# Performance work log

Hardware: AMD Instinct MI355X
Metric: run time of the kernel (lower is better)

The kernel has to match this reference:

```python
import jax, jax.numpy as jnp
import numpy as np

B, T, C, H = 2, 2048, 1024, 16
HS = C // H  # head size = 64


def _rope_cos_sin(t, hs):
    # theta_i = 1/10000^(2(i-1)/hs) for i in [1, hs/2]
    pos = jnp.arange(t, dtype=jnp.float32)[:, None]          # [T,1]
    i = jnp.arange(1, hs // 2 + 1, dtype=jnp.float32)[None]  # [1,hs/2]
    theta = 1.0 / 10000.0 ** (2.0 * (i - 1.0) / hs)
    ang = pos * theta                                        # [T,hs/2]
    return jnp.cos(ang), jnp.sin(ang)


def _apply_rope(u, cos, sin):
    # u: [B,H,T,HS]; complex multiply on consecutive pairs
    u2 = u.reshape(*u.shape[:-1], HS // 2, 2)
    x0, x1 = u2[..., 0], u2[..., 1]
    c = cos[None, None]  # [1,1,T,hs/2]
    s = sin[None, None]
    r0 = x0 * c - x1 * s
    r1 = x0 * s + x1 * c
    return jnp.stack([r0, r1], axis=-1).reshape(u.shape)


def setup_inputs() -> dict:
    key = jax.random.key(0)
    ks = jax.random.split(key, 5)
    return {
        "x": jax.random.normal(ks[0], (B, T, C), dtype=jnp.float32),
        "W_qkv": jax.random.normal(ks[1], (C, 3 * C), dtype=jnp.float32) * 0.02,
        "b_qkv": jax.random.normal(ks[2], (3 * C,), dtype=jnp.float32) * 0.02,
        "W_proj": jax.random.normal(ks[3], (C, C), dtype=jnp.float32) * 0.02,
        "b_proj": jax.random.normal(ks[4], (C,), dtype=jnp.float32) * 0.02,
    }


def reference(x, W_qkv, b_qkv, W_proj, b_proj):
    b, t, c = x.shape
    qkv = x @ W_qkv + b_qkv                                   # [B,T,3C]
    qkv = qkv.reshape(b, t, H, 3 * HS).transpose(0, 2, 1, 3)  # [B,H,T,3*HS]
    q, k, v = jnp.split(qkv, 3, axis=-1)                      # each [B,H,T,HS]

    cos, sin = _rope_cos_sin(t, HS)
    q = _apply_rope(q, cos, sin)
    k = _apply_rope(k, cos, sin)

    att = jnp.einsum("bhqd,bhkd->bhqk", q, k) / jnp.sqrt(jnp.float32(HS))
    causal = jnp.tril(jnp.ones((t, t), dtype=bool))[None, None]
    att = jnp.where(causal, att, jnp.float32(-1e9))
    att = jax.nn.softmax(att, axis=-1)
    y = jnp.einsum("bhqk,bhkd->bhqd", att, v)                 # [B,H,T,HS]
    y = y.transpose(0, 2, 1, 3).reshape(b, t, c)
    return y @ W_proj + b_proj
```

## Files before the change

### kernel.cpp

```cpp
#include <hip/hip_runtime.h>

typedef unsigned short u16;
typedef unsigned int u32;
typedef __bf16 bf16x8 __attribute__((ext_vector_type(8)));
typedef float f32x4 __attribute__((ext_vector_type(4)));
typedef u16 u16x4 __attribute__((ext_vector_type(4)));
typedef u16 u16x8 __attribute__((ext_vector_type(8)));

__device__ __forceinline__ u16 f2bf(float f) {
  u32 u = __builtin_bit_cast(u32, f);
  u += 0x7fffu + ((u >> 16) & 1u);
  return (u16)(u >> 16);
}

__device__ __forceinline__ u32 pk2(float a, float b) {
  u32 ua = __builtin_bit_cast(u32, a) + 0x8000u;
  u32 ub = __builtin_bit_cast(u32, b) + 0x8000u;
  return __builtin_amdgcn_perm(ub, ua, 0x07060302);
}

__device__ __forceinline__ void gld16(const void* g, void* l) {
  __builtin_amdgcn_global_load_lds(
      (const __attribute__((address_space(1))) void*)g,
      (__attribute__((address_space(3))) void*)l, 16, 0, 0);
}

__global__ __launch_bounds__(256) void k_prep(
    const float* __restrict__ x, u16* __restrict__ xb,
    const float* __restrict__ Wqkv, u16* __restrict__ Wqkvt,
    const float* __restrict__ Wproj, u16* __restrict__ Wpt,
    float2* __restrict__ rope) {
  __shared__ float tile[32][33];
  const int tid = threadIdx.x;
  int bx = blockIdx.x;
  if (bx < 4096) {
    int i = (bx * 256 + tid) * 4;
    float4 v = *(const float4*)(x + i);
    u16x4 o = { f2bf(v.x), f2bf(v.y), f2bf(v.z), f2bf(v.w) };
    *(u16x4*)(xb + i) = o;
    return;
  }
  bx -= 4096;
  const float* src; u16* dst; int R, Cc, bxx, byy;
  if (bx < 3072) {
    src = Wqkv; dst = Wqkvt; R = 1024; Cc = 3072; bxx = bx % 96; byy = bx / 96;
  } else if (bx < 4096) {
    int b = bx - 3072;
    src = Wproj; dst = Wpt; R = 1024; Cc = 1024; bxx = b % 32; byy = b / 32;
  } else {
    int i = (bx - 4096) * 256 + tid;
    int t = i >> 5, d = i & 31;
    float theta = expf(-(float)d * 0.28782313662425575f);
    float ang = (float)t * theta;
    rope[i] = make_float2(cosf(ang), sinf(ang));
    return;
  }
  int xx = tid & 31, yy = tid >> 5;
  int c0 = bxx * 32, r0 = byy * 32;
  for (int i = 0; i < 4; ++i)
    tile[yy + 8 * i][xx] = src[(size_t)(r0 + yy + 8 * i) * Cc + c0 + xx];
  __syncthreads();
  for (int i = 0; i < 4; ++i)
    dst[(size_t)(c0 + yy + 8 * i) * R + r0 + xx] = f2bf(tile[xx][yy + 8 * i]);
}

__global__ __launch_bounds__(256, 4) void k_qkv(
    const u16* __restrict__ Xb,
    const u16* __restrict__ Wt,
    const float* __restrict__ bias,
    const float2* __restrict__ rope,
    u16* __restrict__ Qg,
    u16* __restrict__ Kg,
    u16* __restrict__ Vt) {
  __shared__ alignas(16) u16 smem[18432];
  u16* As = smem;
  u16* Bs = smem + 8192;
  const int tid = threadIdx.x;
  const int lane = tid & 63, w = tid >> 6;
  const int quad = lane >> 4, l15 = lane & 15;
  const int m0 = blockIdx.y * 128, n0 = blockIdx.x * 128;
  const int wm = (w & 1) * 64, wn = (w >> 1) * 64;
  const int srow = lane >> 3, sj = lane & 7;
  const int sw = (sj ^ srow) * 8;
  const f32x4 vzero = {0.f, 0.f, 0.f, 0.f};

  f32x4 acc[4][4];
  for (int i = 0; i < 4; ++i)
    for (int j = 0; j < 4; ++j) acc[i][j] = vzero;

  for (int kt = 0; kt < 1024; kt += 64) {
    __syncthreads();
    for (int i = 0; i < 4; ++i) {
      int row = w * 32 + i * 8;
      gld16(Xb + (size_t)(m0 + row + srow) * 1024 + kt + sw, &As[row * 64]);
      gld16(Wt + (size_t)(n0 + row + srow) * 1024 + kt + sw, &Bs[row * 64]);
    }
    __syncthreads();
    for (int ks = 0; ks < 2; ++ks) {
      const int cc = ((ks * 4 + quad) ^ (l15 & 7)) * 8;
      bf16x8 a[4], b[4];
      for (int mt = 0; mt < 4; ++mt)
        a[mt] = *(const bf16x8*)&As[(wm + mt * 16 + l15) * 64 + cc];
      for (int nt = 0; nt < 4; ++nt)
        b[nt] = *(const bf16x8*)&Bs[(wn + nt * 16 + l15) * 64 + cc];
      for (int nt = 0; nt < 4; ++nt)
        for (int mt = 0; mt < 4; ++mt)
          acc[nt][mt] = __builtin_amdgcn_mfma_f32_16x16x32_bf16(
              b[nt], a[mt], acc[nt][mt], 0, 0, 0);
    }
  }
  __syncthreads();

  const int half = w >> 1;
  const int nh = n0 + half * 64;
  const int region = (nh % 192) >> 6;
  u16* Eh = smem + half * 9216;
  if (region < 2) {
    const float qsc = (region == 0) ? 0.18033688011112042f : 1.0f;
    for (int nt = 0; nt < 4; ++nt) {
      float4 bv4 = *(const float4*)&bias[nh + nt * 16 + quad * 4];
      for (int mt = 0; mt < 4; ++mt) {
        int m_l = wm + mt * 16 + l15;
        int t = (m0 + m_l) & 2047;
        float4 cs = *(const float4*)&rope[t * 32 + nt * 8 + quad * 2];
        float v0 = acc[nt][mt][0] + bv4.x;
        float v1 = acc[nt][mt][1] + bv4.y;
        float v2 = acc[nt][mt][2] + bv4.z;
        float v3 = acc[nt][mt][3] + bv4.w;
        float r0 = fmaf(-v1, cs.y, v0 * cs.x) * qsc;
        float r1 = fmaf( v0, cs.y, v1 * cs.x) * qsc;
        float r2 = fmaf(-v3, cs.w, v2 * cs.z) * qsc;
        float r3 = fmaf( v2, cs.w, v3 * cs.z) * qsc;
        uint2 pv; pv.x = pk2(r0, r1); pv.y = pk2(r2, r3);
        *(uint2*)&Eh[m_l * 72 + nt * 16 + quad * 4] = pv;
      }
    }
  } else {
    for (int nt = 0; nt < 4; ++nt) {
      float4 bv4 = *(const float4*)&bias[nh + nt * 16 + quad * 4];
      for (int mt = 0; mt < 4; ++mt) {
        int m_l = wm + mt * 16 + l15;
        int cb = nt * 16 + quad * 4;
        Eh[(cb + 0) * 136 + m_l] = f2bf(acc[nt][mt][0] + bv4.x);
        Eh[(cb + 1) * 136 + m_l] = f2bf(acc[nt][mt][1] + bv4.y);
        Eh[(cb + 2) * 136 + m_l] = f2bf(acc[nt][mt][2] + bv4.z);
        Eh[(cb + 3) * 136 + m_l] = f2bf(acc[nt][mt][3] + bv4.w);
      }
    }
  }
  __syncthreads();

  const int bb = m0 >> 11, t0 = m0 & 2047;
  for (int hf = 0; hf < 2; ++hf) {
    const int nhf = n0 + hf * 64;
    const int hh = nhf / 192;
    const int reg = (nhf % 192) >> 6;
    const u16* Ef = smem + hf * 9216;
    if (reg < 2) {
      u16* dst = (reg == 0 ? Qg : Kg) +
                 ((size_t)(bb * 16 + hh) * 2048 + t0) * 64;
      int chunk = tid & 7, row0 = tid >> 3;
      for (int p = 0; p < 4; ++p) {
        int row = row0 + p * 32;
        u16x8 val = *(const u16x8*)&Ef[row * 72 + chunk * 8];
        *(u16x8*)(dst + (size_t)row * 64 + chunk * 8) = val;
      }
    } else {
      u16* dstv = Vt + (size_t)(bb * 16 + hh) * 64 * 2048 + t0;
      int mch = tid & 15, c0r = tid >> 4;
      for (int p = 0; p < 4; ++p) {
        int c = c0r + p * 16;
        u16x8 val = *(const u16x8*)&Ef[c * 136 + mch * 8];
        *(u16x8*)(dstv + (size_t)c * 2048 + mch * 8) = val;
      }
    }
  }
}

__global__ __launch_bounds__(256, 4) void k_attn(
    const u16* __restrict__ Qg, const u16* __restrict__ Kg,
    const u16* __restrict__ Vt, u16* __restrict__ Og) {
  __shared__ alignas(16) u16 Ks[2][64 * 64];
  __shared__ alignas(16) u16 Vs[2][64 * 64];
  __shared__ alignas(16) u16 Ps[64 * 64];
  const int tid = threadIdx.x, lane = tid & 63, w = tid >> 6;
  const int quad = lane >> 4, l15 = lane & 15;
  const int id = blockIdx.x;
  const int xr = id & 7, j = id >> 3;
  const int bh = (j >> 5) * 8 + xr;
  const int x32 = (j + 7 * (j >> 5)) & 31;
  const int qt = (x32 & 1) ? (x32 >> 1) : (31 - (x32 >> 1));
  const u16* Qh = Qg + (size_t)bh * 2048 * 64;
  const u16* Kh = Kg + (size_t)bh * 2048 * 64;
  const u16* Vh = Vt + (size_t)bh * 64 * 2048;
  const f32x4 vzero = {0.f, 0.f, 0.f, 0.f};
  const int myrow = w * 16;
  const int bb = bh >> 4, h = bh & 15;

  const int r8 = lane >> 3, j8 = lane & 7;
  const int sw_c = (j8 ^ r8) * 8;
  const int psw = (l15 & 7) << 1;

  for (int i = 0; i < 2; ++i) {
    int row = w * 16 + i * 8;
    gld16(Kh + (size_t)(row + r8) * 64 + sw_c, &Ks[0][row * 64]);
    gld16(Vh + (size_t)(row + r8) * 2048 + sw_c, &Vs[0][row * 64]);
  }

  const int q0 = qt * 64;
  bf16x8 aq[2];
  {
    const u16* qp = Qh + (size_t)(q0 + myrow + l15) * 64 + quad * 8;
    aq[0] = *(const bf16x8*)(qp);
    aq[1] = *(const bf16x8*)(qp + 32);
  }
  float lsum = 0.f;
  f32x4 O[4];
  for (int nt = 0; nt < 4; ++nt) O[nt] = vzero;

  int buf = 0;
  const int nk = qt + 1;
  for (int kb = 0; kb < nk; ++kb) {
    const int k0 = kb * 64;
    __syncthreads();
    if (kb + 1 < nk) {
      const int nxt = k0 + 64;
      for (int i = 0; i < 2; ++i) {
        int row = w * 16 + i * 8;
        gld16(Kh + (size_t)(nxt + row + r8) * 64 + sw_c, &Ks[buf ^ 1][row * 64]);
        gld16(Vh + (size_t)(row + r8) * 2048 + nxt + sw_c, &Vs[buf ^ 1][row * 64]);
      }
    }

    f32x4 st[4];
    for (int nt = 0; nt < 4; ++nt) st[nt] = vzero;
    for (int ks = 0; ks < 2; ++ks) {
      bf16x8 ak[4];
      for (int nt = 0; nt < 4; ++nt)
        ak[nt] = *(const bf16x8*)&Ks[buf][(nt * 16 + l15) * 64 +
                                         ((ks * 4 + quad) ^ (l15 & 7)) * 8];
      for (int nt = 0; nt < 4; ++nt)
        st[nt] = __builtin_amdgcn_mfma_f32_16x16x32_bf16(ak[nt], aq[ks], st[nt], 0, 0, 0);
    }

    const int prow = myrow + l15;
    if (kb < qt) {
      for (int nt = 0; nt < 4; ++nt) {
        float p0 = __builtin_amdgcn_exp2f(st[nt][0]);
        float p1 = __builtin_amdgcn_exp2f(st[nt][1]);
        float p2 = __builtin_amdgcn_exp2f(st[nt][2]);
        float p3 = __builtin_amdgcn_exp2f(st[nt][3]);
        lsum += (p0 + p1) + (p2 + p3);
        uint2 pv; pv.x = pk2(p0, p1); pv.y = pk2(p2, p3);
        *(uint2*)&Ps[prow * 64 + ((nt * 4 + quad) ^ psw) * 4] = pv;
      }
    } else {
      const int tq = q0 + myrow + l15;
      const int kbase = k0 + quad * 4;
      for (int nt = 0; nt < 4; ++nt) {
        float p[4];
        for (int r = 0; r < 4; ++r) {
          float pv = __builtin_amdgcn_exp2f(st[nt][r]);
          p[r] = (kbase + nt * 16 + r <= tq) ? pv : 0.f;
          lsum += p[r];
        }
        uint2 pv; pv.x = pk2(p[0], p[1]); pv.y = pk2(p[2], p[3]);
        *(uint2*)&Ps[prow * 64 + ((nt * 4 + quad) ^ psw) * 4] = pv;
      }
    }

    for (int ks = 0; ks < 2; ++ks) {
      bf16x8 a = *(const bf16x8*)&Ps[prow * 64 + ((ks * 8 + quad * 2) ^ psw) * 4];
      bf16x8 bv[4];
      for (int nt = 0; nt < 4; ++nt)
        bv[nt] = *(const bf16x8*)&Vs[buf][(nt * 16 + l15) * 64 +
                                         ((ks * 4 + quad) ^ (l15 & 7)) * 8];
      for (int nt = 0; nt < 4; ++nt)
        O[nt] = __builtin_amdgcn_mfma_f32_16x16x32_bf16(a, bv[nt], O[nt], 0, 0, 0);
    }
    buf ^= 1;
  }

  float ls = lsum;
  ls += __shfl_xor(ls, 16, 64);
  ls += __shfl_xor(ls, 32, 64);
  float inv[4];
  for (int r = 0; r < 4; ++r)
    inv[r] = 1.0f / __shfl(ls, quad * 4 + r, 16);

  for (int nt = 0; nt < 4; ++nt)
    for (int r = 0; r < 4; ++r) {
      int row = myrow + quad * 4 + r;
      int col = nt * 16 + l15;
      int up = (col >> 2) ^ ((row & 7) << 1);
      Ps[row * 64 + up * 4 + (col & 3)] = f2bf(O[nt][r] * inv[r]);
    }
  __syncthreads();
  u16* dst = Og + ((size_t)bb * 2048 + q0) * 1024 + h * 64;
  int chunk = tid & 7, row0 = tid >> 3;
  for (int p = 0; p < 2; ++p) {
    int row = row0 + p * 32;
    int up = (chunk * 2) ^ ((row & 7) << 1);
    u16x8 val = *(const u16x8*)&Ps[row * 64 + up * 4];
    *(u16x8*)(dst + (size_t)row * 1024 + chunk * 8) = val;
  }
}

__global__ __launch_bounds__(256, 4) void k_proj(
    const u16* __restrict__ Ag,
    const u16* __restrict__ Wt,
    const float* __restrict__ bias,
    float* __restrict__ out) {
  __shared__ alignas(16) u16 As[64 * 64];
  __shared__ alignas(16) u16 Bs[128 * 64];
  const int tid = threadIdx.x;
  const int lane = tid & 63, w = tid >> 6;
  const int quad = lane >> 4, l15 = lane & 15;
  const int m0 = blockIdx.y * 64, n0 = blockIdx.x * 128;
  const int wm = (w & 1) * 32, wn = (w >> 1) * 64;
  const int srow = lane >> 3, sj = lane & 7;
  const int sw = (sj ^ srow) * 8;
  const f32x4 vzero = {0.f, 0.f, 0.f, 0.f};

  f32x4 acc[2][4];
  for (int i = 0; i < 2; ++i)
    for (int j = 0; j < 4; ++j) acc[i][j] = vzero;

  for (int kt = 0; kt < 1024; kt += 64) {
    __syncthreads();
    for (int i = 0; i < 2; ++i) {
      int row = w * 16 + i * 8;
      gld16(Ag + (size_t)(m0 + row + srow) * 1024 + kt + sw, &As[row * 64]);
    }
    for (int i = 0; i < 4; ++i) {
      int row = w * 32 + i * 8;
      gld16(Wt + (size_t)(n0 + row + srow) * 1024 + kt + sw, &Bs[row * 64]);
    }
    __syncthreads();
    for (int ks = 0; ks < 2; ++ks) {
      const int cc = ((ks * 4 + quad) ^ (l15 & 7)) * 8;
      bf16x8 a[2], b[4];
      for (int mt = 0; mt < 2; ++mt)
        a[mt] = *(const bf16x8*)&As[(wm + mt * 16 + l15) * 64 + cc];
      for (int nt = 0; nt < 4; ++nt)
        b[nt] = *(const bf16x8*)&Bs[(wn + nt * 16 + l15) * 64 + cc];
      for (int mt = 0; mt < 2; ++mt)
        for (int nt = 0; nt < 4; ++nt)
          acc[mt][nt] = __builtin_amdgcn_mfma_f32_16x16x32_bf16(
              a[mt], b[nt], acc[mt][nt], 0, 0, 0);
    }
  }

  for (int nt = 0; nt < 4; ++nt) {
    int n = n0 + wn + nt * 16 + l15;
    float bv = bias[n];
    for (int mt = 0; mt < 2; ++mt)
      for (int r = 0; r < 4; ++r) {
        int m = m0 + wm + mt * 16 + quad * 4 + r;
        out[(size_t)m * 1024 + n] = acc[mt][nt][r] + bv;
      }
  }
}

extern "C" void kernel_launch(void* const* d_in, const int* in_sizes, int n_in,
                              void* d_out, int out_size, void* d_ws, size_t ws_size,
                              hipStream_t stream) {
  (void)in_sizes; (void)n_in; (void)out_size; (void)ws_size;
  const float* x     = (const float*)d_in[0];
  const float* Wqkv  = (const float*)d_in[1];
  const float* bqkv  = (const float*)d_in[2];
  const float* Wproj = (const float*)d_in[3];
  const float* bproj = (const float*)d_in[4];
  float* out = (float*)d_out;

  char* ws = (char*)d_ws;
  size_t off = 0;
  u16* Xb    = (u16*)(ws + off); off += (size_t)4096 * 1024 * 2;
  u16* Wqkvt = (u16*)(ws + off); off += (size_t)3072 * 1024 * 2;
  u16* Wpt   = (u16*)(ws + off); off += (size_t)1024 * 1024 * 2;
  u16* Qg    = (u16*)(ws + off); off += (size_t)2 * 16 * 2048 * 64 * 2;
  u16* Kg    = (u16*)(ws + off); off += (size_t)2 * 16 * 2048 * 64 * 2;
  u16* Vt    = (u16*)(ws + off); off += (size_t)2 * 16 * 64 * 2048 * 2;
  u16* Att   = (u16*)(ws + off); off += (size_t)4096 * 1024 * 2;
  float2* rope = (float2*)(ws + off); off += (size_t)2048 * 32 * sizeof(float2);

  k_prep<<<8448, 256, 0, stream>>>(x, Xb, Wqkv, Wqkvt, Wproj, Wpt, rope);
  k_qkv<<<dim3(24, 32), 256, 0, stream>>>(Xb, Wqkvt, bqkv, rope, Qg, Kg, Vt);
  k_attn<<<1024, 256, 0, stream>>>(Qg, Kg, Vt, Att);
  k_proj<<<dim3(8, 64), 256, 0, stream>>>(Att, Wpt, bproj, out);
}
```

Before: 175.7 us.

## Pair complementary causal query tiles per block to share K/V loads

Each attention block now processes two query tiles, qA and 31-qA, in one pass over the key blocks. Each K/V tile staged in LDS serves both tiles, and every block does the same total causal work, which balances load across a grid halved to 512 blocks. The cost is doubled accumulator registers and a second P buffer in LDS. Launch bounds drop to 2 waves per SIMD, so occupancy is lower.

```diff
diff --git a/kernel.cpp b/kernel.cpp
--- a/kernel.cpp
+++ b/kernel.cpp
@@ -177,19 +177,21 @@
   }
 }
 
-__global__ __launch_bounds__(256, 4) void k_attn(
+__global__ __launch_bounds__(256, 2) void k_attn(
     const u16* __restrict__ Qg, const u16* __restrict__ Kg,
     const u16* __restrict__ Vt, u16* __restrict__ Og) {
   __shared__ alignas(16) u16 Ks[2][64 * 64];
   __shared__ alignas(16) u16 Vs[2][64 * 64];
-  __shared__ alignas(16) u16 Ps[64 * 64];
+  __shared__ alignas(16) u16 PsA[64 * 64];
+  __shared__ alignas(16) u16 PsB[64 * 64];
   const int tid = threadIdx.x, lane = tid & 63, w = tid >> 6;
   const int quad = lane >> 4, l15 = lane & 15;
   const int id = blockIdx.x;
   const int xr = id & 7, j = id >> 3;
-  const int bh = (j >> 5) * 8 + xr;
-  const int x32 = (j + 7 * (j >> 5)) & 31;
-  const int qt = (x32 & 1) ? (x32 >> 1) : (31 - (x32 >> 1));
+  const int bh = (j >> 4) * 8 + xr;
+  const int p15 = j & 15;
+  const int bx = (j >> 5) ? (15 - p15) : p15;
+  const int qA = bx, qB = 31 - bx;
   const u16* Qh = Qg + (size_t)bh * 2048 * 64;
   const u16* Kh = Kg + (size_t)bh * 2048 * 64;
   const u16* Vh = Vt + (size_t)bh * 64 * 2048;
@@ -200,6 +202,7 @@
   const int r8 = lane >> 3, j8 = lane & 7;
   const int sw_c = (j8 ^ r8) * 8;
   const int psw = (l15 & 7) << 1;
+  const int prow = myrow + l15;
 
   for (int i = 0; i < 2; ++i) {
     int row = w * 16 + i * 8;
@@ -207,23 +210,26 @@
     gld16(Vh + (size_t)(row + r8) * 2048 + sw_c, &Vs[0][row * 64]);
   }
 
-  const int q0 = qt * 64;
-  bf16x8 aq[2];
+  const int q0A = qA * 64, q0B = qB * 64;
+  bf16x8 aqA[2], aqB[2];
   {
-    const u16* qp = Qh + (size_t)(q0 + myrow + l15) * 64 + quad * 8;
-    aq[0] = *(const bf16x8*)(qp);
-    aq[1] = *(const bf16x8*)(qp + 32);
-  }
-  float lsum = 0.f;
-  f32x4 O[4];
-  for (int nt = 0; nt < 4; ++nt) O[nt] = vzero;
+    const u16* qpA = Qh + (size_t)(q0A + prow) * 64 + quad * 8;
+    aqA[0] = *(const bf16x8*)(qpA);
+    aqA[1] = *(const bf16x8*)(qpA + 32);
+    const u16* qpB = Qh + (size_t)(q0B + prow) * 64 + quad * 8;
+    aqB[0] = *(const bf16x8*)(qpB);
+    aqB[1] = *(const bf16x8*)(qpB + 32);
+  }
+  float lsumA = 0.f, lsumB = 0.f;
+  f32x4 OA[4], OB[4];
+  for (int nt = 0; nt < 4; ++nt) { OA[nt] = vzero; OB[nt] = vzero; }
 
   int buf = 0;
-  const int nk = qt + 1;
-  for (int kb = 0; kb < nk; ++kb) {
+  for (int kb = 0; kb <= qB; ++kb) {
     const int k0 = kb * 64;
+    const bool dA = (kb <= qA);
     __syncthreads();
-    if (kb + 1 < nk) {
+    if (kb < qB) {
       const int nxt = k0 + 64;
       for (int i = 0; i < 2; ++i) {
         int row = w * 16 + i * 8;
@@ -232,77 +238,119 @@
       }
     }
 
-    f32x4 st[4];
-    for (int nt = 0; nt < 4; ++nt) st[nt] = vzero;
+    f32x4 stA[4], stB[4];
+    for (int nt = 0; nt < 4; ++nt) { stA[nt] = vzero; stB[nt] = vzero; }
     for (int ks = 0; ks < 2; ++ks) {
       bf16x8 ak[4];
       for (int nt = 0; nt < 4; ++nt)
         ak[nt] = *(const bf16x8*)&Ks[buf][(nt * 16 + l15) * 64 +
                                          ((ks * 4 + quad) ^ (l15 & 7)) * 8];
       for (int nt = 0; nt < 4; ++nt)
-        st[nt] = __builtin_amdgcn_mfma_f32_16x16x32_bf16(ak[nt], aq[ks], st[nt], 0, 0, 0);
-    }
-
-    const int prow = myrow + l15;
-    if (kb < qt) {
+        stB[nt] = __builtin_amdgcn_mfma_f32_16x16x32_bf16(ak[nt], aqB[ks], stB[nt], 0, 0, 0);
+      if (dA)
+        for (int nt = 0; nt < 4; ++nt)
+          stA[nt] = __builtin_amdgcn_mfma_f32_16x16x32_bf16(ak[nt], aqA[ks], stA[nt], 0, 0, 0);
+    }
+
+    if (dA) {
+      if (kb < qA) {
+        for (int nt = 0; nt < 4; ++nt) {
+          float p0 = __builtin_amdgcn_exp2f(stA[nt][0]);
+          float p1 = __builtin_amdgcn_exp2f(stA[nt][1]);
+          float p2 = __builtin_amdgcn_exp2f(stA[nt][2]);
+          float p3 = __builtin_amdgcn_exp2f(stA[nt][3]);
+          lsumA += (p0 + p1) + (p2 + p3);
+          uint2 pv; pv.x = pk2(p0, p1); pv.y = pk2(p2, p3);
+          *(uint2*)&PsA[prow * 64 + ((nt * 4 + quad) ^ psw) * 4] = pv;
+        }
+      } else {
+        const int tq = q0A + prow;
+        const int kbase = k0 + quad * 4;
+        for (int nt = 0; nt < 4; ++nt) {
+          float p[4];
+          for (int r = 0; r < 4; ++r) {
+            float pv = __builtin_amdgcn_exp2f(stA[nt][r]);
+            p[r] = (kbase + nt * 16 + r <= tq) ? pv : 0.f;
+            lsumA += p[r];
+          }
+          uint2 pv; pv.x = pk2(p[0], p[1]); pv.y = pk2(p[2], p[3]);
+          *(uint2*)&PsA[prow * 64 + ((nt * 4 + quad) ^ psw) * 4] = pv;
+        }
+      }
+    }
+    if (kb < qB) {
       for (int nt = 0; nt < 4; ++nt) {
-        float p0 = __builtin_amdgcn_exp2f(st[nt][0]);
-        float p1 = __builtin_amdgcn_exp2f(st[nt][1]);
-        float p2 = __builtin_amdgcn_exp2f(st[nt][2]);
-        float p3 = __builtin_amdgcn_exp2f(st[nt][3]);
-        lsum += (p0 + p1) + (p2 + p3);
+        float p0 = __builtin_amdgcn_exp2f(stB[nt][0]);
+        float p1 = __builtin_amdgcn_exp2f(stB[nt][1]);
+        float p2 = __builtin_amdgcn_exp2f(stB[nt][2]);
+        float p3 = __builtin_amdgcn_exp2f(stB[nt][3]);
+        lsumB += (p0 + p1) + (p2 + p3);
         uint2 pv; pv.x = pk2(p0, p1); pv.y = pk2(p2, p3);
-        *(uint2*)&Ps[prow * 64 + ((nt * 4 + quad) ^ psw) * 4] = pv;
+        *(uint2*)&PsB[prow * 64 + ((nt * 4 + quad) ^ psw) * 4] = pv;
       }
     } else {
-      const int tq = q0 + myrow + l15;
+      const int tq = q0B + prow;
       const int kbase = k0 + quad * 4;
       for (int nt = 0; nt < 4; ++nt) {
         float p[4];
         for (int r = 0; r < 4; ++r) {
-          float pv = __builtin_amdgcn_exp2f(st[nt][r]);
+          float pv = __builtin_amdgcn_exp2f(stB[nt][r]);
           p[r] = (kbase + nt * 16 + r <= tq) ? pv : 0.f;
-          lsum += p[r];
+          lsumB += p[r];
         }
         uint2 pv; pv.x = pk2(p[0], p[1]); pv.y = pk2(p[2], p[3]);
-        *(uint2*)&Ps[prow * 64 + ((nt * 4 + quad) ^ psw) * 4] = pv;
+        *(uint2*)&PsB[prow * 64 + ((nt * 4 + quad) ^ psw) * 4] = pv;
       }
     }
 
     for (int ks = 0; ks < 2; ++ks) {
-      bf16x8 a = *(const bf16x8*)&Ps[prow * 64 + ((ks * 8 + quad * 2) ^ psw) * 4];
       bf16x8 bv[4];
       for (int nt = 0; nt < 4; ++nt)
         bv[nt] = *(const bf16x8*)&Vs[buf][(nt * 16 + l15) * 64 +
                                          ((ks * 4 + quad) ^ (l15 & 7)) * 8];
-      for (int nt = 0; nt < 4; ++nt)
-        O[nt] = __builtin_amdgcn_mfma_f32_16x16x32_bf16(a, bv[nt], O[nt], 0, 0, 0);
+      bf16x8 aB = *(const bf16x8*)&PsB[prow * 64 + ((ks * 8 + quad * 2) ^ psw) * 4];
+      for (int nt = 0; nt < 4; ++nt)
+        OB[nt] = __builtin_amdgcn_mfma_f32_16x16x32_bf16(aB, bv[nt], OB[nt], 0, 0, 0);
+      if (dA) {
+        bf16x8 aA = *(const bf16x8*)&PsA[prow * 64 + ((ks * 8 + quad * 2) ^ psw) * 4];
+        for (int nt = 0; nt < 4; ++nt)
+          OA[nt] = __builtin_amdgcn_mfma_f32_16x16x32_bf16(aA, bv[nt], OA[nt], 0, 0, 0);
+      }
     }
     buf ^= 1;
   }
 
-  float ls = lsum;
-  ls += __shfl_xor(ls, 16, 64);
-  ls += __shfl_xor(ls, 32, 64);
-  float inv[4];
-  for (int r = 0; r < 4; ++r)
-    inv[r] = 1.0f / __shfl(ls, quad * 4 + r, 16);
+  float lsA = lsumA;
+  lsA += __shfl_xor(lsA, 16, 64);
+  lsA += __shfl_xor(lsA, 32, 64);
+  float lsB = lsumB;
+  lsB += __shfl_xor(lsB, 16, 64);
+  lsB += __shfl_xor(lsB, 32, 64);
+  float invA[4], invB[4];
+  for (int r = 0; r < 4; ++r) {
+    invA[r] = 1.0f / __shfl(lsA, quad * 4 + r, 16);
+    invB[r] = 1.0f / __shfl(lsB, quad * 4 + r, 16);
+  }
 
   for (int nt = 0; nt < 4; ++nt)
     for (int r = 0; r < 4; ++r) {
       int row = myrow + quad * 4 + r;
       int col = nt * 16 + l15;
       int up = (col >> 2) ^ ((row & 7) << 1);
-      Ps[row * 64 + up * 4 + (col & 3)] = f2bf(O[nt][r] * inv[r]);
+      PsA[row * 64 + up * 4 + (col & 3)] = f2bf(OA[nt][r] * invA[r]);
+      PsB[row * 64 + up * 4 + (col & 3)] = f2bf(OB[nt][r] * invB[r]);
     }
   __syncthreads();
-  u16* dst = Og + ((size_t)bb * 2048 + q0) * 1024 + h * 64;
+  u16* dstA = Og + ((size_t)bb * 2048 + q0A) * 1024 + h * 64;
+  u16* dstB = Og + ((size_t)bb * 2048 + q0B) * 1024 + h * 64;
   int chunk = tid & 7, row0 = tid >> 3;
   for (int p = 0; p < 2; ++p) {
     int row = row0 + p * 32;
     int up = (chunk * 2) ^ ((row & 7) << 1);
-    u16x8 val = *(const u16x8*)&Ps[row * 64 + up * 4];
-    *(u16x8*)(dst + (size_t)row * 1024 + chunk * 8) = val;
+    u16x8 vA = *(const u16x8*)&PsA[row * 64 + up * 4];
+    *(u16x8*)(dstA + (size_t)row * 1024 + chunk * 8) = vA;
+    u16x8 vB = *(const u16x8*)&PsB[row * 64 + up * 4];
+    *(u16x8*)(dstB + (size_t)row * 1024 + chunk * 8) = vB;
   }
 }
 
@@ -386,6 +434,6 @@
 
   k_prep<<<8448, 256, 0, stream>>>(x, Xb, Wqkv, Wqkvt, Wproj, Wpt, rope);
   k_qkv<<<dim3(24, 32), 256, 0, stream>>>(Xb, Wqkvt, bqkv, rope, Qg, Kg, Vt);
-  k_attn<<<1024, 256, 0, stream>>>(Qg, Kg, Vt, Att);
+  k_attn<<<512, 256, 0, stream>>>(Qg, Kg, Vt, Att);
   k_proj<<<dim3(8, 64), 256, 0, stream>>>(Att, Wpt, bproj, out);
 }
```

New measurement: 169.8 us. -3.4%, faster.

## Split attention work per wave across paired 16-row strips and key halves

Applied to the files above, without the earlier changes.

Restructures the attention kernel so each wave handles two 16-row query strips (s and 127-s), split into halves of the key range between wave pairs, and merges partial outputs and row sums through shared memory. K and V fragments are now loaded straight from global memory into registers instead of being double-buffered through LDS, which removes the per-iteration block barriers. The aim is balanced causal work across waves and fewer syncs. The cost is more global and L2 traffic, because each wave reloads K/V, plus an extra cross-wave reduction.

```diff
diff --git a/kernel.cpp b/kernel.cpp
--- a/kernel.cpp
+++ b/kernel.cpp
@@ -177,74 +177,46 @@
   }
 }
 
-__global__ __launch_bounds__(256, 4) void k_attn(
-    const u16* __restrict__ Qg, const u16* __restrict__ Kg,
-    const u16* __restrict__ Vt, u16* __restrict__ Og) {
-  __shared__ alignas(16) u16 Ks[2][64 * 64];
-  __shared__ alignas(16) u16 Vs[2][64 * 64];
-  __shared__ alignas(16) u16 Ps[64 * 64];
-  const int tid = threadIdx.x, lane = tid & 63, w = tid >> 6;
-  const int quad = lane >> 4, l15 = lane & 15;
-  const int id = blockIdx.x;
-  const int xr = id & 7, j = id >> 3;
-  const int bh = (j >> 5) * 8 + xr;
-  const int x32 = (j + 7 * (j >> 5)) & 31;
-  const int qt = (x32 & 1) ? (x32 >> 1) : (31 - (x32 >> 1));
-  const u16* Qh = Qg + (size_t)bh * 2048 * 64;
-  const u16* Kh = Kg + (size_t)bh * 2048 * 64;
-  const u16* Vh = Vt + (size_t)bh * 64 * 2048;
+__device__ __forceinline__ float sub_attn(
+    const u16* __restrict__ Qh, const u16* __restrict__ Kh,
+    const u16* __restrict__ Vh, u16* Psw,
+    int su, int lo, int hi, int quad, int l15, int psw, f32x4 (&O)[4]) {
   const f32x4 vzero = {0.f, 0.f, 0.f, 0.f};
-  const int myrow = w * 16;
-  const int bb = bh >> 4, h = bh & 15;
-
-  const int r8 = lane >> 3, j8 = lane & 7;
-  const int sw_c = (j8 ^ r8) * 8;
-  const int psw = (l15 & 7) << 1;
-
-  for (int i = 0; i < 2; ++i) {
-    int row = w * 16 + i * 8;
-    gld16(Kh + (size_t)(row + r8) * 64 + sw_c, &Ks[0][row * 64]);
-    gld16(Vh + (size_t)(row + r8) * 2048 + sw_c, &Vs[0][row * 64]);
-  }
-
-  const int q0 = qt * 64;
+  for (int nt = 0; nt < 4; ++nt) O[nt] = vzero;
+  float lsum = 0.f;
   bf16x8 aq[2];
   {
-    const u16* qp = Qh + (size_t)(q0 + myrow + l15) * 64 + quad * 8;
+    const u16* qp = Qh + (size_t)(su * 16 + l15) * 64 + quad * 8;
     aq[0] = *(const bf16x8*)(qp);
     aq[1] = *(const bf16x8*)(qp + 32);
   }
-  float lsum = 0.f;
-  f32x4 O[4];
-  for (int nt = 0; nt < 4; ++nt) O[nt] = vzero;
-
-  int buf = 0;
-  const int nk = qt + 1;
-  for (int kb = 0; kb < nk; ++kb) {
+  const int nkm1 = su >> 2;
+  const int tq = su * 16 + l15;
+  for (int kb = lo; kb < hi; ++kb) {
     const int k0 = kb * 64;
-    __syncthreads();
-    if (kb + 1 < nk) {
-      const int nxt = k0 + 64;
-      for (int i = 0; i < 2; ++i) {
-        int row = w * 16 + i * 8;
-        gld16(Kh + (size_t)(nxt + row + r8) * 64 + sw_c, &Ks[buf ^ 1][row * 64]);
-        gld16(Vh + (size_t)(row + r8) * 2048 + nxt + sw_c, &Vs[buf ^ 1][row * 64]);
-      }
-    }
-
+    bf16x8 ak[4][2];
+    {
+      const u16* kp = Kh + (size_t)(k0 + l15) * 64 + quad * 8;
+      for (int nt = 0; nt < 4; ++nt)
+        for (int ks = 0; ks < 2; ++ks)
+          ak[nt][ks] = *(const bf16x8*)(kp + nt * 1024 + ks * 32);
+    }
     f32x4 st[4];
     for (int nt = 0; nt < 4; ++nt) st[nt] = vzero;
-    for (int ks = 0; ks < 2; ++ks) {
-      bf16x8 ak[4];
-      for (int nt = 0; nt < 4; ++nt)
-        ak[nt] = *(const bf16x8*)&Ks[buf][(nt * 16 + l15) * 64 +
-                                         ((ks * 4 + quad) ^ (l15 & 7)) * 8];
-      for (int nt = 0; nt < 4; ++nt)
-        st[nt] = __builtin_amdgcn_mfma_f32_16x16x32_bf16(ak[nt], aq[ks], st[nt], 0, 0, 0);
-    }
-
-    const int prow = myrow + l15;
-    if (kb < qt) {
+    for (int ks = 0; ks < 2; ++ks)
+      for (int nt = 0; nt < 4; ++nt)
+        st[nt] = __builtin_amdgcn_mfma_f32_16x16x32_bf16(
+            ak[nt][ks], aq[ks], st[nt], 0, 0, 0);
+
+    bf16x8 bv[4][2];
+    {
+      const u16* vp = Vh + (size_t)l15 * 2048 + k0 + quad * 8;
+      for (int nt = 0; nt < 4; ++nt)
+        for (int ks = 0; ks < 2; ++ks)
+          bv[nt][ks] = *(const bf16x8*)(vp + (size_t)nt * 32768 + ks * 32);
+    }
+
+    if (kb < nkm1) {
       for (int nt = 0; nt < 4; ++nt) {
         float p0 = __builtin_amdgcn_exp2f(st[nt][0]);
         float p1 = __builtin_amdgcn_exp2f(st[nt][1]);
@@ -252,10 +224,9 @@
         float p3 = __builtin_amdgcn_exp2f(st[nt][3]);
         lsum += (p0 + p1) + (p2 + p3);
         uint2 pv; pv.x = pk2(p0, p1); pv.y = pk2(p2, p3);
-        *(uint2*)&Ps[prow * 64 + ((nt * 4 + quad) ^ psw) * 4] = pv;
+        *(uint2*)&Psw[l15 * 64 + ((nt * 4 + quad) ^ psw) * 4] = pv;
       }
     } else {
-      const int tq = q0 + myrow + l15;
       const int kbase = k0 + quad * 4;
       for (int nt = 0; nt < 4; ++nt) {
         float p[4];
@@ -265,44 +236,97 @@
           lsum += p[r];
         }
         uint2 pv; pv.x = pk2(p[0], p[1]); pv.y = pk2(p[2], p[3]);
-        *(uint2*)&Ps[prow * 64 + ((nt * 4 + quad) ^ psw) * 4] = pv;
+        *(uint2*)&Psw[l15 * 64 + ((nt * 4 + quad) ^ psw) * 4] = pv;
       }
     }
 
     for (int ks = 0; ks < 2; ++ks) {
-      bf16x8 a = *(const bf16x8*)&Ps[prow * 64 + ((ks * 8 + quad * 2) ^ psw) * 4];
-      bf16x8 bv[4];
-      for (int nt = 0; nt < 4; ++nt)
-        bv[nt] = *(const bf16x8*)&Vs[buf][(nt * 16 + l15) * 64 +
-                                         ((ks * 4 + quad) ^ (l15 & 7)) * 8];
-      for (int nt = 0; nt < 4; ++nt)
-        O[nt] = __builtin_amdgcn_mfma_f32_16x16x32_bf16(a, bv[nt], O[nt], 0, 0, 0);
-    }
-    buf ^= 1;
-  }
-
-  float ls = lsum;
-  ls += __shfl_xor(ls, 16, 64);
-  ls += __shfl_xor(ls, 32, 64);
-  float inv[4];
-  for (int r = 0; r < 4; ++r)
-    inv[r] = 1.0f / __shfl(ls, quad * 4 + r, 16);
-
-  for (int nt = 0; nt < 4; ++nt)
-    for (int r = 0; r < 4; ++r) {
-      int row = myrow + quad * 4 + r;
-      int col = nt * 16 + l15;
-      int up = (col >> 2) ^ ((row & 7) << 1);
-      Ps[row * 64 + up * 4 + (col & 3)] = f2bf(O[nt][r] * inv[r]);
-    }
+      bf16x8 pa = *(const bf16x8*)&Psw[l15 * 64 + ((ks * 8 + quad * 2) ^ psw) * 4];
+      for (int nt = 0; nt < 4; ++nt)
+        O[nt] = __builtin_amdgcn_mfma_f32_16x16x32_bf16(
+            pa, bv[nt][ks], O[nt], 0, 0, 0);
+    }
+  }
+  lsum += __shfl_xor(lsum, 16, 64);
+  lsum += __shfl_xor(lsum, 32, 64);
+  return lsum;
+}
+
+__global__ __launch_bounds__(256, 4) void k_attn(
+    const u16* __restrict__ Qg, const u16* __restrict__ Kg,
+    const u16* __restrict__ Vt, u16* __restrict__ Og) {
+  __shared__ alignas(16) u16 Ps[4][1024];
+  __shared__ alignas(16) float MO[4][1024];
+  __shared__ float ML[4][16];
+  const int tid = threadIdx.x, lane = tid & 63, w = tid >> 6;
+  const int quad = lane >> 4, l15 = lane & 15;
+  const int id = blockIdx.x;
+  const int xcd = id & 7, g = id >> 3;
+  const int bh = (g >> 5) * 8 + xcd;
+  const int gg = g & 31;
+  const int sp = 2 * gg + (w >> 1);
+  const int s1 = sp, s2 = 127 - sp;
+  const int hhf = w & 1;
+  const int nk1 = (s1 >> 2) + 1, nk2 = (s2 >> 2) + 1;
+  const int c1 = nk1 >> 1, c2 = nk2 >> 1;
+  const int lo1 = hhf ? c1 : 0, hi1 = hhf ? nk1 : c1;
+  const int lo2 = hhf ? c2 : 0, hi2 = hhf ? nk2 : c2;
+  const u16* Qh = Qg + (size_t)bh * 2048 * 64;
+  const u16* Kh = Kg + (size_t)bh * 2048 * 64;
+  const u16* Vh = Vt + (size_t)bh * 64 * 2048;
+  u16* Psw = Ps[w];
+  const int psw = (l15 & 7) << 1;
+
+  f32x4 O1[4], O2[4];
+  const float ls1 = sub_attn(Qh, Kh, Vh, Psw, s1, lo1, hi1, quad, l15, psw, O1);
+  const float ls2 = sub_attn(Qh, Kh, Vh, Psw, s2, lo2, hi2, quad, l15, psw, O2);
+
+  if (w & 1) {
+    for (int nt = 0; nt < 4; ++nt)
+      for (int r = 0; r < 4; ++r)
+        MO[w][(quad * 4 + r) * 64 + nt * 16 + l15] = O1[nt][r];
+    if (lane < 16) ML[w][l15] = ls1;
+  } else {
+    for (int nt = 0; nt < 4; ++nt)
+      for (int r = 0; r < 4; ++r)
+        MO[w][(quad * 4 + r) * 64 + nt * 16 + l15] = O2[nt][r];
+    if (lane < 16) ML[w][l15] = ls2;
+  }
   __syncthreads();
-  u16* dst = Og + ((size_t)bb * 2048 + q0) * 1024 + h * 64;
-  int chunk = tid & 7, row0 = tid >> 3;
+
+  const int sm = (w & 1) ? s2 : s1;
+  {
+    float lsm = ((w & 1) ? ls2 : ls1) + ML[w ^ 1][l15];
+    float inv[4];
+    for (int r = 0; r < 4; ++r)
+      inv[r] = 1.0f / __shfl(lsm, quad * 4 + r, 16);
+    if (w & 1) {
+      for (int nt = 0; nt < 4; ++nt)
+        for (int r = 0; r < 4; ++r) {
+          float o = O2[nt][r] + MO[w ^ 1][(quad * 4 + r) * 64 + nt * 16 + l15];
+          int row = quad * 4 + r, col = nt * 16 + l15;
+          int up = (col >> 2) ^ ((row & 7) << 1);
+          Psw[row * 64 + up * 4 + (col & 3)] = f2bf(o * inv[r]);
+        }
+    } else {
+      for (int nt = 0; nt < 4; ++nt)
+        for (int r = 0; r < 4; ++r) {
+          float o = O1[nt][r] + MO[w ^ 1][(quad * 4 + r) * 64 + nt * 16 + l15];
+          int row = quad * 4 + r, col = nt * 16 + l15;
+          int up = (col >> 2) ^ ((row & 7) << 1);
+          Psw[row * 64 + up * 4 + (col & 3)] = f2bf(o * inv[r]);
+        }
+    }
+  }
+
+  const int bb = bh >> 4, h = bh & 15;
+  u16* dst = Og + ((size_t)bb * 2048 + sm * 16) * 1024 + h * 64;
+  const int rrow = lane >> 2, ch4 = lane & 3;
   for (int p = 0; p < 2; ++p) {
-    int row = row0 + p * 32;
-    int up = (chunk * 2) ^ ((row & 7) << 1);
-    u16x8 val = *(const u16x8*)&Ps[row * 64 + up * 4];
-    *(u16x8*)(dst + (size_t)row * 1024 + chunk * 8) = val;
+    int chunk = ch4 + p * 4;
+    int up = (chunk * 2) ^ ((rrow & 7) << 1);
+    u16x8 val = *(const u16x8*)&Psw[rrow * 64 + up * 4];
+    *(u16x8*)(dst + (size_t)rrow * 1024 + chunk * 8) = val;
   }
 }
 
```

Result: slower. 252.4 us (+43.7%).

## Pair complementary causal query tiles per attention block with a two-deep prefetch pipeline

Applied to the files above, without the earlier changes.

Each attention workgroup now processes two query tiles, qt and 31-qt, so every block does exactly 33 key-block iterations and the causal triangle is balanced without a scheduling permutation. The grid is halved to 512 blocks. The K/V staging moves to a two-stage prefetch using explicit vmcnt waits and raw s_barrier in place of __syncthreads. The first tile's output is normalised and written mid-loop. This trades fewer, longer, uniform blocks (possibly lower occupancy fill across CUs) for removing tail imbalance and exposing more load latency hiding; the hand-written waitcnt logic carries correctness risk.

```diff
diff --git a/kernel.cpp b/kernel.cpp
--- a/kernel.cpp
+++ b/kernel.cpp
@@ -187,9 +187,8 @@
   const int quad = lane >> 4, l15 = lane & 15;
   const int id = blockIdx.x;
   const int xr = id & 7, j = id >> 3;
-  const int bh = (j >> 5) * 8 + xr;
-  const int x32 = (j + 7 * (j >> 5)) & 31;
-  const int qt = (x32 & 1) ? (x32 >> 1) : (31 - (x32 >> 1));
+  const int bx = j & 15;
+  const int bh = (j >> 4) * 8 + xr;
   const u16* Qh = Qg + (size_t)bh * 2048 * 64;
   const u16* Kh = Kg + (size_t)bh * 2048 * 64;
   const u16* Vh = Vt + (size_t)bh * 64 * 2048;
@@ -197,53 +196,67 @@
   const int myrow = w * 16;
   const int bb = bh >> 4, h = bh & 15;
 
+  const int qA = bx, qB = 31 - bx;
+  const int nkA = qA + 1;
+  const int q0A = qA * 64, q0B = qB * 64;
+
   const int r8 = lane >> 3, j8 = lane & 7;
   const int sw_c = (j8 ^ r8) * 8;
   const int psw = (l15 & 7) << 1;
-
-  for (int i = 0; i < 2; ++i) {
-    int row = w * 16 + i * 8;
-    gld16(Kh + (size_t)(row + r8) * 64 + sw_c, &Ks[0][row * 64]);
-    gld16(Vh + (size_t)(row + r8) * 2048 + sw_c, &Vs[0][row * 64]);
-  }
-
-  const int q0 = qt * 64;
-  bf16x8 aq[2];
+  const int prow = myrow + l15;
+
+  bf16x8 aqA[2], aqB[2];
   {
-    const u16* qp = Qh + (size_t)(q0 + myrow + l15) * 64 + quad * 8;
-    aq[0] = *(const bf16x8*)(qp);
-    aq[1] = *(const bf16x8*)(qp + 32);
-  }
+    const u16* qpA = Qh + (size_t)(q0A + prow) * 64 + quad * 8;
+    aqA[0] = *(const bf16x8*)(qpA);
+    aqA[1] = *(const bf16x8*)(qpA + 32);
+    const u16* qpB = Qh + (size_t)(q0B + prow) * 64 + quad * 8;
+    aqB[0] = *(const bf16x8*)(qpB);
+    aqB[1] = *(const bf16x8*)(qpB + 32);
+  }
+  asm volatile("" ::: "memory");
+
+  auto stage = [&](int i, int b) {
+    const int kk0 = (i < nkA ? i : i - nkA) * 64;
+    for (int t = 0; t < 2; ++t) {
+      int row = w * 16 + t * 8;
+      gld16(Kh + (size_t)(kk0 + row + r8) * 64 + sw_c, &Ks[b][row * 64]);
+      gld16(Vh + (size_t)(row + r8) * 2048 + kk0 + sw_c, &Vs[b][row * 64]);
+    }
+  };
+  stage(0, 0);
+  stage(1, 1);
+
   float lsum = 0.f;
   f32x4 O[4];
   for (int nt = 0; nt < 4; ++nt) O[nt] = vzero;
 
-  int buf = 0;
-  const int nk = qt + 1;
-  for (int kb = 0; kb < nk; ++kb) {
+  for (int it = 0; it < 33; ++it) {
+    const int buf = it & 1;
+    if (it == 32) asm volatile("s_waitcnt vmcnt(0)" ::: "memory");
+    else          asm volatile("s_waitcnt vmcnt(4)" ::: "memory");
+    asm volatile("s_barrier" ::: "memory");
+
+    const bool isA = it < nkA;
+    const int kb = isA ? it : it - nkA;
     const int k0 = kb * 64;
-    __syncthreads();
-    if (kb + 1 < nk) {
-      const int nxt = k0 + 64;
-      for (int i = 0; i < 2; ++i) {
-        int row = w * 16 + i * 8;
-        gld16(Kh + (size_t)(nxt + row + r8) * 64 + sw_c, &Ks[buf ^ 1][row * 64]);
-        gld16(Vh + (size_t)(row + r8) * 2048 + nxt + sw_c, &Vs[buf ^ 1][row * 64]);
-      }
-    }
+    const int qt = isA ? qA : qB;
+    const int q0 = isA ? q0A : q0B;
+    const bf16x8 q0f = isA ? aqA[0] : aqB[0];
+    const bf16x8 q1f = isA ? aqA[1] : aqB[1];
 
     f32x4 st[4];
     for (int nt = 0; nt < 4; ++nt) st[nt] = vzero;
     for (int ks = 0; ks < 2; ++ks) {
+      const bf16x8 qf = ks ? q1f : q0f;
       bf16x8 ak[4];
       for (int nt = 0; nt < 4; ++nt)
         ak[nt] = *(const bf16x8*)&Ks[buf][(nt * 16 + l15) * 64 +
                                          ((ks * 4 + quad) ^ (l15 & 7)) * 8];
       for (int nt = 0; nt < 4; ++nt)
-        st[nt] = __builtin_amdgcn_mfma_f32_16x16x32_bf16(ak[nt], aq[ks], st[nt], 0, 0, 0);
-    }
-
-    const int prow = myrow + l15;
+        st[nt] = __builtin_amdgcn_mfma_f32_16x16x32_bf16(ak[nt], qf, st[nt], 0, 0, 0);
+    }
+
     if (kb < qt) {
       for (int nt = 0; nt < 4; ++nt) {
         float p0 = __builtin_amdgcn_exp2f(st[nt][0]);
@@ -255,7 +268,7 @@
         *(uint2*)&Ps[prow * 64 + ((nt * 4 + quad) ^ psw) * 4] = pv;
       }
     } else {
-      const int tq = q0 + myrow + l15;
+      const int tq = q0 + prow;
       const int kbase = k0 + quad * 4;
       for (int nt = 0; nt < 4; ++nt) {
         float p[4];
@@ -278,7 +291,37 @@
       for (int nt = 0; nt < 4; ++nt)
         O[nt] = __builtin_amdgcn_mfma_f32_16x16x32_bf16(a, bv[nt], O[nt], 0, 0, 0);
     }
-    buf ^= 1;
+
+    asm volatile("s_barrier" ::: "memory");
+    if (it + 2 < 33) stage(it + 2, buf);
+
+    if (it == nkA - 1) {
+      float ls = lsum;
+      ls += __shfl_xor(ls, 16, 64);
+      ls += __shfl_xor(ls, 32, 64);
+      float inv[4];
+      for (int r = 0; r < 4; ++r)
+        inv[r] = 1.0f / __shfl(ls, quad * 4 + r, 16);
+      for (int nt = 0; nt < 4; ++nt)
+        for (int r = 0; r < 4; ++r) {
+          int row = myrow + quad * 4 + r;
+          int col = nt * 16 + l15;
+          int up = (col >> 2) ^ ((row & 7) << 1);
+          Ps[row * 64 + up * 4 + (col & 3)] = f2bf(O[nt][r] * inv[r]);
+        }
+      asm volatile("s_waitcnt lgkmcnt(0)" ::: "memory");
+      asm volatile("s_barrier" ::: "memory");
+      u16* dst = Og + ((size_t)bb * 2048 + q0A) * 1024 + h * 64;
+      int chunk = tid & 7, row0 = tid >> 3;
+      for (int p = 0; p < 2; ++p) {
+        int row = row0 + p * 32;
+        int up = (chunk * 2) ^ ((row & 7) << 1);
+        u16x8 val = *(const u16x8*)&Ps[row * 64 + up * 4];
+        *(u16x8*)(dst + (size_t)row * 1024 + chunk * 8) = val;
+      }
+      lsum = 0.f;
+      for (int nt = 0; nt < 4; ++nt) O[nt] = vzero;
+    }
   }
 
   float ls = lsum;
@@ -287,7 +330,6 @@
   float inv[4];
   for (int r = 0; r < 4; ++r)
     inv[r] = 1.0f / __shfl(ls, quad * 4 + r, 16);
-
   for (int nt = 0; nt < 4; ++nt)
     for (int r = 0; r < 4; ++r) {
       int row = myrow + quad * 4 + r;
@@ -295,8 +337,9 @@
       int up = (col >> 2) ^ ((row & 7) << 1);
       Ps[row * 64 + up * 4 + (col & 3)] = f2bf(O[nt][r] * inv[r]);
     }
-  __syncthreads();
-  u16* dst = Og + ((size_t)bb * 2048 + q0) * 1024 + h * 64;
+  asm volatile("s_waitcnt lgkmcnt(0)" ::: "memory");
+  asm volatile("s_barrier" ::: "memory");
+  u16* dst = Og + ((size_t)bb * 2048 + q0B) * 1024 + h * 64;
   int chunk = tid & 7, row0 = tid >> 3;
   for (int p = 0; p < 2; ++p) {
     int row = row0 + p * 32;
@@ -386,6 +429,6 @@
 
   k_prep<<<8448, 256, 0, stream>>>(x, Xb, Wqkv, Wqkvt, Wproj, Wpt, rope);
   k_qkv<<<dim3(24, 32), 256, 0, stream>>>(Xb, Wqkvt, bqkv, rope, Qg, Kg, Vt);
-  k_attn<<<1024, 256, 0, stream>>>(Qg, Kg, Vt, Att);
+  k_attn<<<512, 256, 0, stream>>>(Qg, Kg, Vt, Att);
   k_proj<<<dim3(8, 64), 256, 0, stream>>>(Att, Wpt, bproj, out);
 }
```

Result: faster. 171.1 us (-2.6%).
